# Kernel tuning notes

Hardware: AMD Instinct MI355X
Metric: run time of the kernel (lower is better)

Reference implementation:

```python
import jax, jax.numpy as jnp
import numpy as np
from jax import lax

B, C, H, W = 2, 96, 64, 64
D_INNER, D_STATE, DT_RANK, K = 192, 16, 6, 4
EPS = 1e-5


def _ln(x, g, b):
    mu = jnp.mean(x, -1, keepdims=True)
    var = jnp.var(x, -1, keepdims=True)
    return (x - mu) * lax.rsqrt(var + EPS) * g + b


def setup_inputs() -> dict:
    key = jax.random.key(0)
    ks = jax.random.split(key, 10)
    f = lambda k, s, sc=0.02: jax.random.normal(k, s, dtype=jnp.float32) * sc
    return {
        "rgb": jax.random.normal(ks[0], (B, C, H, W), dtype=jnp.float32),
        "t": jax.random.normal(ks[1], (B, C, H, W), dtype=jnp.float32),
        "conv_w": f(ks[2], (C, 2 * C, 3, 3), 0.05),
        "conv_b": jnp.zeros((C,), jnp.float32),
        "bn_gamma": jnp.ones((C,), jnp.float32),
        "bn_beta": jnp.zeros((C,), jnp.float32),
        "bn_mean": jnp.zeros((C,), jnp.float32),
        "bn_var": jnp.ones((C,), jnp.float32),
        "ln_gamma": jnp.ones((C,), jnp.float32),
        "ln_beta": jnp.zeros((C,), jnp.float32),
        "in_proj_w": f(ks[3], (2 * D_INNER, C)),
        "dwconv_w": f(ks[4], (D_INNER, 1, 3, 3), 0.1),
        "dwconv_b": jnp.zeros((D_INNER,), jnp.float32),
        "x_proj_w": f(ks[5], (K, DT_RANK + 2 * D_STATE, D_INNER)),
        "dt_w": f(ks[6], (K, D_INNER, DT_RANK), 0.1),
        "dt_b": jnp.full((K, D_INNER), float(np.log(np.expm1(0.01))), jnp.float32),
        "A_logs": jnp.log(jnp.tile(jnp.arange(1, D_STATE + 1, dtype=jnp.float32), (K * D_INNER, 1))),
        "Ds": jnp.ones((K * D_INNER,), jnp.float32),
        "out_norm_gamma": jnp.ones((D_INNER,), jnp.float32),
        "out_norm_beta": jnp.zeros((D_INNER,), jnp.float32),
        "out_proj_w": f(ks[7], (C, D_INNER)),
    }


def _forward(rgb, t, conv_w, conv_b, bn_gamma, bn_beta, bn_mean, bn_var,
             ln_gamma, ln_beta, in_proj_w, dwconv_w, dwconv_b, x_proj_w,
             dt_w, dt_b, A_logs, Ds, out_norm_gamma, out_norm_beta, out_proj_w):
    dn = ("NCHW", "OIHW", "NCHW")
    # BasicConv: conv + BN(eval) + ReLU (dropout inactive in eval)
    x = jnp.concatenate([rgb, t], axis=1)
    x = lax.conv_general_dilated(x, conv_w, (1, 1), "SAME", dimension_numbers=dn)
    x = x + conv_b[None, :, None, None]
    x = (x - bn_mean[None, :, None, None]) * lax.rsqrt(bn_var[None, :, None, None] + EPS)
    x = x * bn_gamma[None, :, None, None] + bn_beta[None, :, None, None]
    x = jax.nn.relu(x)
    # permute to (B,H,W,C) and LayerNorm over channels
    x = _ln(jnp.transpose(x, (0, 2, 3, 1)), ln_gamma, ln_beta)
    # ---- SS2D ----
    xz = jnp.einsum("bhwc,ec->bhwe", x, in_proj_w)  # e = 2*d_inner
    xc, z = jnp.split(xz, 2, axis=-1)
    xc = jnp.transpose(xc, (0, 3, 1, 2))  # (B, d_inner, H, W)
    xc = lax.conv_general_dilated(xc, dwconv_w, (1, 1), "SAME",
                                  dimension_numbers=dn, feature_group_count=D_INNER)
    xc = jax.nn.silu(xc + dwconv_b[None, :, None, None])
    L = H * W
    # cross-scan: row-major, col-major, and their reverses -> (B,4,d,L)
    x_flat = xc.reshape(B, D_INNER, L)
    x_tr = jnp.transpose(xc, (0, 1, 3, 2)).reshape(B, D_INNER, L)
    xs = jnp.stack([x_flat, x_tr], axis=1)
    xs = jnp.concatenate([xs, xs[..., ::-1]], axis=1)  # (B,K,d,L)
    x_dbl = jnp.einsum("bkdl,kcd->bkcl", xs, x_proj_w)
    dts = x_dbl[:, :, :DT_RANK]
    Bs = x_dbl[:, :, DT_RANK:DT_RANK + D_STATE]  # (B,K,N,L)
    Cs = x_dbl[:, :, DT_RANK + D_STATE:]         # (B,K,N,L)
    dts = jnp.einsum("bkrl,kdr->bkdl", dts, dt_w)
    A = -jnp.exp(A_logs).reshape(K, D_INNER, D_STATE)
    Dsk = Ds.reshape(K, D_INNER)
    delta = jax.nn.softplus(dts + dt_b[None, :, :, None])  # (B,K,d,L)
    du = delta * xs

    def step(h, inp):
        dl, dul, Bl, Cl = inp  # (B,K,d),(B,K,d),(B,K,N),(B,K,N)
        h = h * jnp.exp(dl[..., None] * A) + dul[..., None] * Bl[:, :, None, :]
        y = jnp.einsum("bkdn,bkn->bkd", h, Cl)
        return h, y

    h0 = jnp.zeros((B, K, D_INNER, D_STATE), delta.dtype)
    _, ys = lax.scan(step, h0, (
        jnp.transpose(delta, (3, 0, 1, 2)),
        jnp.transpose(du, (3, 0, 1, 2)),
        jnp.transpose(Bs, (3, 0, 1, 2)),
        jnp.transpose(Cs, (3, 0, 1, 2)),
    ))
    out_y = jnp.transpose(ys, (1, 2, 3, 0)) + xs * Dsk[None, :, :, None]  # (B,K,d,L)
    # merge four scan directions back to row-major order
    inv_y = out_y[:, 2:4, :, ::-1]
    wh_y = jnp.transpose(out_y[:, 1].reshape(B, D_INNER, W, H), (0, 1, 3, 2)).reshape(B, D_INNER, L)
    invwh_y = jnp.transpose(inv_y[:, 1].reshape(B, D_INNER, W, H), (0, 1, 3, 2)).reshape(B, D_INNER, L)
    y = out_y[:, 0] + inv_y[:, 0] + wh_y + invwh_y  # (B,d,L)
    y = jnp.transpose(y, (0, 2, 1)).reshape(B, H, W, D_INNER)
    y = _ln(y, out_norm_gamma, out_norm_beta)
    y = y * jax.nn.silu(z)
    out = jnp.einsum("bhwd,cd->bhwc", y, out_proj_w)
    return jnp.transpose(out, (0, 3, 1, 2))  # (B,C,H,W)


def reference(rgb, t, conv_w, conv_b, bn_gamma, bn_beta, bn_mean, bn_var,
              ln_gamma, ln_beta, in_proj_w, dwconv_w, dwconv_b, x_proj_w,
              dt_w, dt_b, A_logs, Ds, out_norm_gamma, out_norm_beta, out_proj_w):
    return _forward(rgb, t, conv_w, conv_b, bn_gamma, bn_beta, bn_mean, bn_var,
                    ln_gamma, ln_beta, in_proj_w, dwconv_w, dwconv_b, x_proj_w,
                    dt_w, dt_b, A_logs, Ds, out_norm_gamma, out_norm_beta, out_proj_w)
```

## Files before the change

### kernel.cpp

```cpp
#include <hip/hip_runtime.h>
#include <math.h>

#define HW 4096
#define CC 96
#define DD 192
#define NS 16
#define KK 4
#define LC 64
#define NC 64
#define NCH (8*DD*NS)

__device__ __forceinline__ float siluf(float x){ return x / (1.f + expf(-x)); }
__device__ __forceinline__ float softplusf(float x){ return (x > 20.f) ? x : log1pf(expf(x)); }

__device__ __forceinline__ int lmap_xs(int k, int l){
  if (k == 1) return ((l & 63) << 6) | (l >> 6);
  if (k == 2) return (HW - 1) - l;
  if (k == 3) { int r = (HW - 1) - l; return ((r & 63) << 6) | (r >> 6); }
  return l;
}

__global__ void __launch_bounds__(512, 2)
k_conv1(const float* __restrict__ rgb, const float* __restrict__ tt,
        const float* __restrict__ cw, float* __restrict__ pbuf){
  __shared__ float in_lds[8][10][68];
  __shared__ float w_lds[8][9][48];
  int bi = blockIdx.x;
  int kc  = bi & 7;        int ci0 = kc*24;
  int r2  = bi >> 3;
  int cog = r2 & 1;        int co0 = cog*48;
  int r3  = r2 >> 1;
  int b   = r3 & 1;
  int pt  = r3 >> 1;       int h0 = pt*8;
  int tid = threadIdx.x;
  int pg = tid & 63;  int r = pg >> 3;  int w0 = (pg & 7)*8;
  int cg = tid >> 6;  int co_t = cg*6;

  float acc[6][8];
  #pragma unroll
  for (int c = 0; c < 6; ++c)
    #pragma unroll
    for (int p = 0; p < 8; ++p) acc[c][p] = 0.f;

  for (int s = 0; s < 3; ++s){
    if (s) __syncthreads();
    for (int i = tid; i < 80; i += 512){ in_lds[i/10][i%10][0] = 0.f; in_lds[i/10][i%10][65] = 0.f; }
    for (int i = tid; i < 5120; i += 512){
      int ci = i / 640; int rr = (i % 640) / 64; int w = i & 63;
      int grow = h0 - 1 + rr;
      int cig = ci0 + s*8 + ci;
      float v = 0.f;
      if (grow >= 0 && grow < 64){
        const float* src = (cig < CC) ? (rgb + (size_t)(b*CC+cig)*HW)
                                      : (tt  + (size_t)(b*CC+cig-CC)*HW);
        v = src[grow*64 + w];
      }
      in_lds[ci][rr][w+1] = v;
    }
    for (int i = tid; i < 3456; i += 512){
      int co = i % 48; int rest = i / 48; int ci = rest / 9; int tap = rest % 9;
      int cig = ci0 + s*8 + ci;
      w_lds[ci][tap][co] = cw[((size_t)(co0+co)*192 + cig)*9 + tap];
    }
    __syncthreads();
    #pragma unroll
    for (int ci = 0; ci < 8; ++ci){
      float rowv[3][10];
      #pragma unroll
      for (int rr = 0; rr < 3; ++rr){
        const float* rp = &in_lds[ci][r+rr][w0];
        float4 a = *(const float4*)rp;
        float4 bb = *(const float4*)(rp+4);
        float2 cc = *(const float2*)(rp+8);
        rowv[rr][0]=a.x; rowv[rr][1]=a.y; rowv[rr][2]=a.z; rowv[rr][3]=a.w;
        rowv[rr][4]=bb.x; rowv[rr][5]=bb.y; rowv[rr][6]=bb.z; rowv[rr][7]=bb.w;
        rowv[rr][8]=cc.x; rowv[rr][9]=cc.y;
      }
      #pragma unroll
      for (int tap = 0; tap < 9; ++tap){
        int rt = tap/3, ct = tap - rt*3;
        float2 wa = *(const float2*)&w_lds[ci][tap][co_t];
        float2 wb = *(const float2*)&w_lds[ci][tap][co_t+2];
        float2 wc = *(const float2*)&w_lds[ci][tap][co_t+4];
        float wv[6] = {wa.x, wa.y, wb.x, wb.y, wc.x, wc.y};
        #pragma unroll
        for (int p = 0; p < 8; ++p){
          float iv = rowv[rt][p + ct];
          #pragma unroll
          for (int c = 0; c < 6; ++c) acc[c][p] += wv[c]*iv;
        }
      }
    }
  }
  #pragma unroll
  for (int p = 0; p < 8; ++p){
    int pix = (h0 + r)*64 + w0 + p;
    float* o = pbuf + (((size_t)kc*2 + b)*HW + pix)*CC + co0 + co_t;
    float2 o0 = {acc[0][p], acc[1][p]};
    float2 o1 = {acc[2][p], acc[3][p]};
    float2 o2 = {acc[4][p], acc[5][p]};
    *(float2*)&o[0] = o0; *(float2*)&o[2] = o1; *(float2*)&o[4] = o2;
  }
}

__global__ void k_convred(const float* __restrict__ pbuf, const float* __restrict__ cb,
                          const float* __restrict__ bng, const float* __restrict__ bnb,
                          const float* __restrict__ bnm, const float* __restrict__ bnv,
                          const float* __restrict__ lng, const float* __restrict__ lnb,
                          float* __restrict__ xn){
  __shared__ float sm[4], sm2[4], smu[2], srs[2];
  int tid = threadIdx.x;
  int half = tid >> 7;
  int c = tid & 127;
  int pixg = blockIdx.x*2 + half;
  int b = pixg >> 12; int pix = pixg & (HW-1);
  float v = 0.f;
  if (c < CC){
    #pragma unroll
    for (int kc = 0; kc < 8; ++kc)
      v += pbuf[(((size_t)kc*2 + b)*HW + pix)*CC + c];
    v += cb[c];
    v = (v - bnm[c]) * rsqrtf(bnv[c] + 1e-5f);
    v = v * bng[c] + bnb[c];
    v = fmaxf(v, 0.f);
  }
  float s = v, s2 = v*v;
  #pragma unroll
  for (int off = 32; off; off >>= 1){ s += __shfl_down(s, off); s2 += __shfl_down(s2, off); }
  if ((tid & 63) == 0){ sm[tid>>6] = s; sm2[tid>>6] = s2; }
  __syncthreads();
  if (tid < 2){
    float ts = sm[2*tid] + sm[2*tid+1];
    float ts2 = sm2[2*tid] + sm2[2*tid+1];
    float mu = ts * (1.f/CC);
    float var = ts2 * (1.f/CC) - mu*mu;
    smu[tid] = mu; srs[tid] = rsqrtf(var + 1e-5f);
  }
  __syncthreads();
  if (c < CC)
    xn[(size_t)pixg*CC + c] = (v - smu[half])*srs[half]*lng[c] + lnb[c];
}

__global__ void k_inproj(const float* __restrict__ xn, const float* __restrict__ ipw,
                         float* __restrict__ xz){
  __shared__ float As[64][97];
  __shared__ __align__(16) float Bs[96][68];
  int p0 = blockIdx.x*64;
  int e0 = blockIdx.y*64;
  int tid = threadIdx.x;
  for (int idx = tid; idx < 64*96; idx += 256){
    int r = idx/96, c = idx - r*96;
    As[r][c] = xn[(size_t)(p0+r)*96 + c];
  }
  for (int idx = tid; idx < 96*64; idx += 256){
    int c = idx/64, e = idx - c*64;
    Bs[c][e] = ipw[(size_t)(e0+e)*96 + c];
  }
  __syncthreads();
  int tx = tid & 15, ty = tid >> 4;
  float acc[4][4] = {};
  for (int c = 0; c < 96; ++c){
    float a[4];
    #pragma unroll
    for (int i = 0; i < 4; ++i) a[i] = As[ty*4+i][c];
    float4 bb = *(const float4*)&Bs[c][tx*4];
    float bv[4] = {bb.x, bb.y, bb.z, bb.w};
    #pragma unroll
    for (int i = 0; i < 4; ++i)
      #pragma unroll
      for (int j = 0; j < 4; ++j) acc[i][j] += a[i]*bv[j];
  }
  for (int i = 0; i < 4; ++i){
    float4 o = {acc[i][0], acc[i][1], acc[i][2], acc[i][3]};
    *(float4*)&xz[(size_t)(p0+ty*4+i)*384 + e0 + tx*4] = o;
  }
}

__global__ void k_dwconv(const float* __restrict__ xz, const float* __restrict__ dww,
                         const float* __restrict__ dwb, float* __restrict__ xc){
  int tid = blockIdx.x*256 + threadIdx.x;
  int d  = tid % DD;
  int bp = tid / DD;
  int pix = bp & (HW-1); int b = bp >> 12;
  int h = pix >> 6, w = pix & 63;
  float acc = dwb[d];
  #pragma unroll
  for (int dh = -1; dh <= 1; ++dh){
    int hh = h + dh;
    if (hh < 0 || hh > 63) continue;
    #pragma unroll
    for (int dw = -1; dw <= 1; ++dw){
      int ww = w + dw;
      if (ww < 0 || ww > 63) continue;
      acc += xz[((size_t)b*HW + hh*64 + ww)*384 + d] * dww[d*9 + (dh+1)*3 + (dw+1)];
    }
  }
  xc[(size_t)bp*DD + d] = siluf(acc);
}

__global__ void k_xdbl(const float* __restrict__ xc, const float* __restrict__ xpw,
                       const float* __restrict__ dtw, const float* __restrict__ dtb,
                       float* __restrict__ Bsb, float* __restrict__ Csb,
                       float* __restrict__ dlt){
  __shared__ float xs_t[8][194];
  __shared__ float wl[38*194];
  __shared__ float dts_t[8][38];
  int blk = blockIdx.x;
  int lc = blk & 511; int k = (blk >> 9) & 3; int b = blk >> 11;
  int l0 = lc*8;
  int tid = threadIdx.x;
  for (int idx = tid; idx < 38*192; idx += 256){
    int c = idx/192, d = idx - c*192;
    wl[c*194 + d] = xpw[(size_t)(k*38 + c)*192 + d];
  }
  for (int idx = tid; idx < 8*192; idx += 256){
    int li = idx/192, d = idx - li*192;
    int lm = lmap_xs(k, l0 + li);
    xs_t[li][d] = xc[((size_t)b*HW + lm)*DD + d];
  }
  __syncthreads();
  int b4k = b*KK + k;
  for (int o = tid; o < 8*38; o += 256){
    int li = o/38, c = o - li*38;
    const float* wrow = &wl[c*194];
    float s = 0.f;
    #pragma unroll 4
    for (int d = 0; d < 192; ++d) s += xs_t[li][d]*wrow[d];
    int l = l0 + li;
    if (c < 6)       dts_t[li][c] = s;
    else if (c < 22) Bsb[((size_t)b4k*HW + l)*NS + (c-6)]  = s;
    else             Csb[((size_t)b4k*HW + l)*NS + (c-22)] = s;
  }
  __syncthreads();
  for (int o = tid; o < 8*192; o += 256){
    int li = o/192, d = o - li*192;
    int l = l0 + li;
    float s = dtb[k*DD + d];
    #pragma unroll
    for (int r = 0; r < 6; ++r) s += dts_t[li][r]*dtw[(size_t)(k*DD+d)*6 + r];
    dlt[((size_t)b4k*HW + l)*DD + d] = softplusf(s);
  }
}

__global__ void k_scan1(const float* __restrict__ dlt, const float* __restrict__ xc,
                        const float* __restrict__ Bsb, const float* __restrict__ Alog,
                        float* __restrict__ Ac, float* __restrict__ Bc){
  int tid = blockIdx.x*256 + threadIdx.x;
  int ng = tid & 3;
  int t2 = tid >> 2;
  int d = t2 % DD;
  int rest = t2 / DD;
  int chunk = rest & (NC-1);
  int b4k = rest >> 6;
  int k = b4k & 3, b = b4k >> 2;
  float4 Af = *(const float4*)&Alog[(size_t)(k*DD+d)*NS + ng*4];
  float Av[4] = {-expf(Af.x), -expf(Af.y), -expf(Af.z), -expf(Af.w)};
  float h[4] = {0.f,0.f,0.f,0.f};
  float ap[4] = {1.f,1.f,1.f,1.f};
  int l0 = chunk*LC;
  const float* dp  = dlt + ((size_t)b4k*HW + l0)*DD + d;
  const float4* Bp4 = (const float4*)(Bsb + ((size_t)b4k*HW + l0)*NS) + ng;
  const float* xcb = xc + (size_t)b*HW*DD + d;
  float dvc = dp[0];
  float xvc = xcb[(size_t)lmap_xs(k, l0)*DD];
  float4 Bvc = Bp4[0];
  #pragma unroll 4
  for (int i = 0; i < LC; ++i){
    float dvn = 0.f, xvn = 0.f; float4 Bvn = {0.f,0.f,0.f,0.f};
    if (i+1 < LC){
      dvn = dp[(size_t)(i+1)*DD];
      xvn = xcb[(size_t)lmap_xs(k, l0+i+1)*DD];
      Bvn = Bp4[(size_t)(i+1)*4];
    }
    float du = dvc*xvc;
    float a0 = __expf(dvc*Av[0]), a1 = __expf(dvc*Av[1]),
          a2 = __expf(dvc*Av[2]), a3 = __expf(dvc*Av[3]);
    h[0] = h[0]*a0 + du*Bvc.x; ap[0] *= a0;
    h[1] = h[1]*a1 + du*Bvc.y; ap[1] *= a1;
    h[2] = h[2]*a2 + du*Bvc.z; ap[2] *= a2;
    h[3] = h[3]*a3 + du*Bvc.w; ap[3] *= a3;
    dvc = dvn; xvc = xvn; Bvc = Bvn;
  }
  size_t base = (size_t)chunk*NCH + (size_t)(b4k*DD + d)*NS + ng*4;
  *(float4*)&Ac[base] = make_float4(ap[0],ap[1],ap[2],ap[3]);
  *(float4*)&Bc[base] = make_float4(h[0],h[1],h[2],h[3]);
}

__global__ void k_scan2(float* __restrict__ Ac, const float* __restrict__ Bc){
  int chain = blockIdx.x*256 + threadIdx.x;
  float h = 0.f;
  for (int c = 0; c < NC; ++c){
    size_t idx = (size_t)c*NCH + chain;
    float a = Ac[idx], bv = Bc[idx];
    Ac[idx] = h;
    h = a*h + bv;
  }
}

__global__ void k_scan3(const float* __restrict__ dlt, const float* __restrict__ xc,
                        const float* __restrict__ Bsb, const float* __restrict__ Csb,
                        const float* __restrict__ Alog, const float* __restrict__ hst,
                        float* __restrict__ ys){
  int tid = blockIdx.x*256 + threadIdx.x;
  int ng = tid & 3;
  int t2 = tid >> 2;
  int d = t2 % DD;
  int rest = t2 / DD;
  int chunk = rest & (NC-1);
  int b4k = rest >> 6;
  int k = b4k & 3, b = b4k >> 2;
  float4 Af = *(const float4*)&Alog[(size_t)(k*DD+d)*NS + ng*4];
  float Av[4] = {-expf(Af.x), -expf(Af.y), -expf(Af.z), -expf(Af.w)};
  size_t hbase = (size_t)chunk*NCH + (size_t)(b4k*DD + d)*NS + ng*4;
  float4 hf = *(const float4*)&hst[hbase];
  float h[4] = {hf.x, hf.y, hf.z, hf.w};
  int l0 = chunk*LC;
  const float* dp  = dlt + ((size_t)b4k*HW + l0)*DD + d;
  const float4* Bp4 = (const float4*)(Bsb + ((size_t)b4k*HW + l0)*NS) + ng;
  const float4* Cp4 = (const float4*)(Csb + ((size_t)b4k*HW + l0)*NS) + ng;
  const float* xcb = xc + (size_t)b*HW*DD + d;
  float* yp = ys + ((size_t)b4k*HW + l0)*DD + d;
  float dvc = dp[0];
  float xvc = xcb[(size_t)lmap_xs(k, l0)*DD];
  float4 Bvc = Bp4[0];
  float4 Cvc = Cp4[0];
  #pragma unroll 4
  for (int i = 0; i < LC; ++i){
    float dvn = 0.f, xvn = 0.f; float4 Bvn = {0.f,0.f,0.f,0.f}, Cvn = {0.f,0.f,0.f,0.f};
    if (i+1 < LC){
      dvn = dp[(size_t)(i+1)*DD];
      xvn = xcb[(size_t)lmap_xs(k, l0+i+1)*DD];
      Bvn = Bp4[(size_t)(i+1)*4];
      Cvn = Cp4[(size_t)(i+1)*4];
    }
    float du = dvc*xvc;
    float a0 = __expf(dvc*Av[0]), a1 = __expf(dvc*Av[1]),
          a2 = __expf(dvc*Av[2]), a3 = __expf(dvc*Av[3]);
    h[0] = h[0]*a0 + du*Bvc.x;
    h[1] = h[1]*a1 + du*Bvc.y;
    h[2] = h[2]*a2 + du*Bvc.z;
    h[3] = h[3]*a3 + du*Bvc.w;
    float y = h[0]*Cvc.x + h[1]*Cvc.y + h[2]*Cvc.z + h[3]*Cvc.w;
    y += __shfl_xor(y, 1, 4);
    y += __shfl_xor(y, 2, 4);
    if (ng == 0) yp[(size_t)i*DD] = y;
    dvc = dvn; xvc = xvn; Bvc = Bvn; Cvc = Cvn;
  }
}

__global__ void k_gate(const float* __restrict__ ys, const float* __restrict__ xc,
                       const float* __restrict__ Ds, const float* __restrict__ xz,
                       const float* __restrict__ ong, const float* __restrict__ onb,
                       float* __restrict__ yg){
  int gt = blockIdx.x*256 + threadIdx.x;
  int wave = gt >> 6;
  int lane = gt & 63;
  int b = wave >> 12; int l = wave & (HW-1);
  int l1 = ((l & 63) << 6) | (l >> 6);
  size_t base = (size_t)b*KK*HW*DD;
  float v[3]; float s = 0.f, s2 = 0.f;
  #pragma unroll
  for (int j = 0; j < 3; ++j){
    int d = lane + j*64;
    float t;
    t  = ys[base + ((size_t)0*HW + l        )*DD + d];
    t += ys[base + ((size_t)1*HW + l1       )*DD + d];
    t += ys[base + ((size_t)2*HW + (HW-1-l ))*DD + d];
    t += ys[base + ((size_t)3*HW + (HW-1-l1))*DD + d];
    t += xc[((size_t)b*HW + l)*DD + d] * (Ds[d] + Ds[DD+d] + Ds[2*DD+d] + Ds[3*DD+d]);
    v[j] = t; s += t; s2 += t*t;
  }
  #pragma unroll
  for (int off = 32; off; off >>= 1){ s += __shfl_xor(s, off); s2 += __shfl_xor(s2, off); }
  float mu = s*(1.f/DD);
  float rstd = rsqrtf(s2*(1.f/DD) - mu*mu + 1e-5f);
  #pragma unroll
  for (int j = 0; j < 3; ++j){
    int d = lane + j*64;
    float z = xz[((size_t)b*HW + l)*384 + DD + d];
    float x = (v[j]-mu)*rstd*ong[d] + onb[d];
    yg[(size_t)wave*DD + d] = x * siluf(z);
  }
}

__global__ void k_outproj(const float* __restrict__ yg, const float* __restrict__ opw,
                          float* __restrict__ out){
  __shared__ float yl[48][36];
  __shared__ float wl[48][97];
  int blk = blockIdx.x;
  int b = blk >> 7; int pt = blk & 127;
  int px0 = pt*32;
  int tid = threadIdx.x;
  int pxg = tid & 7;
  int cgi = tid >> 3;
  float acc[4][3] = {};
  for (int k0 = 0; k0 < DD; k0 += 48){
    if (k0) __syncthreads();
    for (int i = tid; i < 32*48; i += 256){
      int r = i/48, k = i - r*48;
      yl[k][r] = yg[((size_t)b*HW + px0 + r)*DD + k0 + k];
    }
    for (int i = tid; i < 96*48; i += 256){
      int c = i/48, k = i - c*48;
      wl[k][c] = opw[(size_t)c*DD + k0 + k];
    }
    __syncthreads();
    #pragma unroll 4
    for (int k = 0; k < 48; ++k){
      float4 yv = *(const float4*)&yl[k][pxg*4];
      float w0 = wl[k][cgi*3], w1 = wl[k][cgi*3+1], w2 = wl[k][cgi*3+2];
      acc[0][0] += yv.x*w0; acc[0][1] += yv.x*w1; acc[0][2] += yv.x*w2;
      acc[1][0] += yv.y*w0; acc[1][1] += yv.y*w1; acc[1][2] += yv.y*w2;
      acc[2][0] += yv.z*w0; acc[2][1] += yv.z*w1; acc[2][2] += yv.z*w2;
      acc[3][0] += yv.w*w0; acc[3][1] += yv.w*w1; acc[3][2] += yv.w*w2;
    }
  }
  #pragma unroll
  for (int j = 0; j < 3; ++j){
    int c = cgi*3 + j;
    float4 o = {acc[0][j], acc[1][j], acc[2][j], acc[3][j]};
    *(float4*)&out[((size_t)b*CC + c)*HW + px0 + pxg*4] = o;
  }
}

extern "C" void kernel_launch(void* const* d_in, const int* in_sizes, int n_in,
                              void* d_out, int out_size, void* d_ws, size_t ws_size,
                              hipStream_t stream) {
  const float* rgb   = (const float*)d_in[0];
  const float* tt    = (const float*)d_in[1];
  const float* cw    = (const float*)d_in[2];
  const float* cb    = (const float*)d_in[3];
  const float* bng   = (const float*)d_in[4];
  const float* bnb   = (const float*)d_in[5];
  const float* bnm   = (const float*)d_in[6];
  const float* bnv   = (const float*)d_in[7];
  const float* lng   = (const float*)d_in[8];
  const float* lnb   = (const float*)d_in[9];
  const float* ipw   = (const float*)d_in[10];
  const float* dww   = (const float*)d_in[11];
  const float* dwb   = (const float*)d_in[12];
  const float* xpw   = (const float*)d_in[13];
  const float* dtw   = (const float*)d_in[14];
  const float* dtb   = (const float*)d_in[15];
  const float* Alog  = (const float*)d_in[16];
  const float* Ds    = (const float*)d_in[17];
  const float* ong   = (const float*)d_in[18];
  const float* onb   = (const float*)d_in[19];
  const float* opw   = (const float*)d_in[20];
  float* out = (float*)d_out;

  float* ws = (float*)d_ws;
  float* xn   = ws + 786432;
  float* xz   = ws + 1572864;
  float* xc   = ws + 4718592;
  float* Bsb  = ws + 6291456;
  float* Csb  = ws + 6815744;
  float* dlt  = ws + 7340032;
  float* ysb  = ws + 13631488;
  float* pbuf = ws + 1572864;
  float* Ac   = ws;
  float* Bc   = ysb;
  float* yg   = ws + 7340032;

  k_conv1<<<256, 512, 0, stream>>>(rgb, tt, cw, pbuf);
  k_convred<<<4096, 256, 0, stream>>>(pbuf, cb, bng, bnb, bnm, bnv, lng, lnb, xn);
  dim3 g2(128, 6);
  k_inproj<<<g2, 256, 0, stream>>>(xn, ipw, xz);
  k_dwconv<<<6144, 256, 0, stream>>>(xz, dww, dwb, xc);
  k_xdbl<<<4096, 256, 0, stream>>>(xc, xpw, dtw, dtb, Bsb, Csb, dlt);
  k_scan1<<<1536, 256, 0, stream>>>(dlt, xc, Bsb, Alog, Ac, Bc);
  k_scan2<<<96, 256, 0, stream>>>(Ac, Bc);
  k_scan3<<<1536, 256, 0, stream>>>(dlt, xc, Bsb, Csb, Alog, Ac, ysb);
  k_gate<<<2048, 256, 0, stream>>>(ysb, xc, Ds, xz, ong, onb, yg);
  k_outproj<<<256, 256, 0, stream>>>(yg, opw, out);
}
```

Baseline: 277.8 us.

## Retile x_proj kernel with register-blocked 32-position tiles and chunked LDS staging

Rewrites the x_proj/dt projection kernel so each block handles 32 sequence positions instead of 8. Each thread computes a 5-channel by 2-position register tile, and the reduction dimension is streamed in 48-wide chunks through transposed LDS buffers loaded with float4. This cuts the per-block reload of the full 38x192 weight matrix and makes better use of each weight load. The dt projection now keeps its dt weights in registers. Block count and size change from 4096x256 to 1024x128, which lowers parallelism per launch.

Result: faster. 258.5 us (-6.9%).

```diff
diff --git a/kernel.cpp b/kernel.cpp
--- a/kernel.cpp
+++ b/kernel.cpp
@@ -198,47 +198,112 @@
   xc[(size_t)bp*DD + d] = siluf(acc);
 }
 
-__global__ void k_xdbl(const float* __restrict__ xc, const float* __restrict__ xpw,
-                       const float* __restrict__ dtw, const float* __restrict__ dtb,
-                       float* __restrict__ Bsb, float* __restrict__ Csb,
-                       float* __restrict__ dlt){
-  __shared__ float xs_t[8][194];
-  __shared__ float wl[38*194];
-  __shared__ float dts_t[8][38];
+__global__ void __launch_bounds__(128)
+k_xdbl(const float* __restrict__ xc, const float* __restrict__ xpw,
+       const float* __restrict__ dtw, const float* __restrict__ dtb,
+       float* __restrict__ Bsb, float* __restrict__ Csb,
+       float* __restrict__ dlt){
+  __shared__ float xs_lds[48*36];
+  __shared__ float w_lds[40*52];
+  __shared__ float dts_lds[32][8];
   int blk = blockIdx.x;
-  int lc = blk & 511; int k = (blk >> 9) & 3; int b = blk >> 11;
-  int l0 = lc*8;
+  int lt = blk & 127; int b4k = blk >> 7;
+  int k = b4k & 3, b = b4k >> 2;
+  int l0 = lt*32;
   int tid = threadIdx.x;
-  for (int idx = tid; idx < 38*192; idx += 256){
-    int c = idx/192, d = idx - c*192;
-    wl[c*194 + d] = xpw[(size_t)(k*38 + c)*192 + d];
-  }
-  for (int idx = tid; idx < 8*192; idx += 256){
-    int li = idx/192, d = idx - li*192;
-    int lm = lmap_xs(k, l0 + li);
-    xs_t[li][d] = xc[((size_t)b*HW + lm)*DD + d];
+  int lg = tid & 15, cg = tid >> 4;
+  int c0 = cg*5;
+  float acc[5][2] = {};
+
+  for (int chunk = 0; chunk < 4; ++chunk){
+    int d0 = chunk*48;
+    if (chunk) __syncthreads();
+    #pragma unroll
+    for (int i = tid; i < 384; i += 128){
+      int q = i >> 5, l = i & 31;
+      int lm = lmap_xs(k, l0 + l);
+      float4 v = *(const float4*)&xc[((size_t)b*HW + lm)*DD + d0 + q*4];
+      xs_lds[(q*4+0)*36 + l] = v.x;
+      xs_lds[(q*4+1)*36 + l] = v.y;
+      xs_lds[(q*4+2)*36 + l] = v.z;
+      xs_lds[(q*4+3)*36 + l] = v.w;
+    }
+    for (int i = tid; i < 456; i += 128){
+      int c = i / 12, q = i - (i/12)*12;
+      float4 v = *(const float4*)&xpw[((size_t)(k*38 + c))*192 + d0 + q*4];
+      *(float4*)&w_lds[c*52 + q*4] = v;
+    }
+    __syncthreads();
+    #pragma unroll 2
+    for (int dq = 0; dq < 12; ++dq){
+      float4 wv[5];
+      #pragma unroll
+      for (int j = 0; j < 5; ++j)
+        wv[j] = *(const float4*)&w_lds[(c0+j)*52 + dq*4];
+      #pragma unroll
+      for (int dd = 0; dd < 4; ++dd){
+        float2 xv = *(const float2*)&xs_lds[(dq*4+dd)*36 + lg*2];
+        #pragma unroll
+        for (int j = 0; j < 5; ++j){
+          float wc = ((const float*)&wv[j])[dd];
+          acc[j][0] += wc * xv.x;
+          acc[j][1] += wc * xv.y;
+        }
+      }
+    }
+  }
+
+  int lA = l0 + lg*2;
+  #pragma unroll
+  for (int j = 0; j < 5; ++j){
+    int c = c0 + j;
+    if (c < 6){
+      dts_lds[lg*2  ][c] = acc[j][0];
+      dts_lds[lg*2+1][c] = acc[j][1];
+    } else if (c < 22){
+      Bsb[((size_t)b4k*HW + lA  )*NS + (c-6)] = acc[j][0];
+      Bsb[((size_t)b4k*HW + lA+1)*NS + (c-6)] = acc[j][1];
+    } else if (c < 38){
+      Csb[((size_t)b4k*HW + lA  )*NS + (c-22)] = acc[j][0];
+      Csb[((size_t)b4k*HW + lA+1)*NS + (c-22)] = acc[j][1];
+    }
   }
   __syncthreads();
-  int b4k = b*KK + k;
-  for (int o = tid; o < 8*38; o += 256){
-    int li = o/38, c = o - li*38;
-    const float* wrow = &wl[c*194];
-    float s = 0.f;
-    #pragma unroll 4
-    for (int d = 0; d < 192; ++d) s += xs_t[li][d]*wrow[d];
-    int l = l0 + li;
-    if (c < 6)       dts_t[li][c] = s;
-    else if (c < 22) Bsb[((size_t)b4k*HW + l)*NS + (c-6)]  = s;
-    else             Csb[((size_t)b4k*HW + l)*NS + (c-22)] = s;
-  }
-  __syncthreads();
-  for (int o = tid; o < 8*192; o += 256){
-    int li = o/192, d = o - li*192;
-    int l = l0 + li;
-    float s = dtb[k*DD + d];
-    #pragma unroll
-    for (int r = 0; r < 6; ++r) s += dts_t[li][r]*dtw[(size_t)(k*DD+d)*6 + r];
-    dlt[((size_t)b4k*HW + l)*DD + d] = softplusf(s);
+
+  float dtw_r0[6], dtw_r1[6], dtw_r2[6];
+  int dv0 = tid % 192, dv1 = (tid + 128) % 192, dv2 = (tid + 256) % 192;
+  float dtb0 = dtb[k*DD + dv0], dtb1 = dtb[k*DD + dv1], dtb2 = dtb[k*DD + dv2];
+  #pragma unroll
+  for (int r = 0; r < 6; ++r){
+    dtw_r0[r] = dtw[((size_t)(k*DD + dv0))*6 + r];
+    dtw_r1[r] = dtw[((size_t)(k*DD + dv1))*6 + r];
+    dtw_r2[r] = dtw[((size_t)(k*DD + dv2))*6 + r];
+  }
+  for (int it3 = 0; it3 < 16; ++it3){
+    {
+      int o = tid + (it3*3+0)*128; int l = o / 192;
+      float4 t0 = *(const float4*)&dts_lds[l][0];
+      float2 t1 = *(const float2*)&dts_lds[l][4];
+      float s = dtb0 + t0.x*dtw_r0[0] + t0.y*dtw_r0[1] + t0.z*dtw_r0[2]
+                     + t0.w*dtw_r0[3] + t1.x*dtw_r0[4] + t1.y*dtw_r0[5];
+      dlt[((size_t)b4k*HW + l0 + l)*DD + dv0] = softplusf(s);
+    }
+    {
+      int o = tid + (it3*3+1)*128; int l = o / 192;
+      float4 t0 = *(const float4*)&dts_lds[l][0];
+      float2 t1 = *(const float2*)&dts_lds[l][4];
+      float s = dtb1 + t0.x*dtw_r1[0] + t0.y*dtw_r1[1] + t0.z*dtw_r1[2]
+                     + t0.w*dtw_r1[3] + t1.x*dtw_r1[4] + t1.y*dtw_r1[5];
+      dlt[((size_t)b4k*HW + l0 + l)*DD + dv1] = softplusf(s);
+    }
+    {
+      int o = tid + (it3*3+2)*128; int l = o / 192;
+      float4 t0 = *(const float4*)&dts_lds[l][0];
+      float2 t1 = *(const float2*)&dts_lds[l][4];
+      float s = dtb2 + t0.x*dtw_r2[0] + t0.y*dtw_r2[1] + t0.z*dtw_r2[2]
+                     + t0.w*dtw_r2[3] + t1.x*dtw_r2[4] + t1.y*dtw_r2[5];
+      dlt[((size_t)b4k*HW + l0 + l)*DD + dv2] = softplusf(s);
+    }
   }
 }
 
@@ -467,7 +532,7 @@
   dim3 g2(128, 6);
   k_inproj<<<g2, 256, 0, stream>>>(xn, ipw, xz);
   k_dwconv<<<6144, 256, 0, stream>>>(xz, dww, dwb, xc);
-  k_xdbl<<<4096, 256, 0, stream>>>(xc, xpw, dtw, dtb, Bsb, Csb, dlt);
+  k_xdbl<<<1024, 128, 0, stream>>>(xc, xpw, dtw, dtb, Bsb, Csb, dlt);
   k_scan1<<<1536, 256, 0, stream>>>(dlt, xc, Bsb, Alog, Ac, Bc);
   k_scan2<<<96, 256, 0, stream>>>(Ac, Bc);
   k_scan3<<<1536, 256, 0, stream>>>(dlt, xc, Bsb, Csb, Alog, Ac, ysb);
```

## Retile x_proj kernel into 64-position blocks with register-blocked 4x4 outer products

Applied to the files above, without the earlier changes.

Rewrites the x_dbl projection kernel so each block handles 64 sequence positions for one (batch, direction) pair instead of 8. The block loads the projection weights in 48-wide chunks into transposed shared memory and computes a 4x4 register tile per thread. The old version reloaded the full 38x192 weight matrix into shared memory for every 8 positions and did scalar dot products. The delta computation now writes contiguous per-position rows and uses a fast exp in softplus, which may slightly change accuracy. Fewer, larger blocks (512 blocks of 192 threads) and about 60KB of shared memory per block could lower occupancy.

Measured after the change: 255.8 us. -7.9%, faster.

```diff
diff --git a/kernel.cpp b/kernel.cpp
--- a/kernel.cpp
+++ b/kernel.cpp
@@ -12,6 +12,7 @@
 
 __device__ __forceinline__ float siluf(float x){ return x / (1.f + expf(-x)); }
 __device__ __forceinline__ float softplusf(float x){ return (x > 20.f) ? x : log1pf(expf(x)); }
+__device__ __forceinline__ float softplus_fast(float x){ return (x > 20.f) ? x : log1pf(__expf(x)); }
 
 __device__ __forceinline__ int lmap_xs(int k, int l){
   if (k == 1) return ((l & 63) << 6) | (l >> 6);
@@ -198,47 +199,95 @@
   xc[(size_t)bp*DD + d] = siluf(acc);
 }
 
-__global__ void k_xdbl(const float* __restrict__ xc, const float* __restrict__ xpw,
-                       const float* __restrict__ dtw, const float* __restrict__ dtb,
-                       float* __restrict__ Bsb, float* __restrict__ Csb,
-                       float* __restrict__ dlt){
-  __shared__ float xs_t[8][194];
-  __shared__ float wl[38*194];
-  __shared__ float dts_t[8][38];
+__global__ void __launch_bounds__(192)
+k_xdbl(const float* __restrict__ xc, const float* __restrict__ xpw,
+       const float* __restrict__ dtw, const float* __restrict__ dtb,
+       float* __restrict__ Bsb, float* __restrict__ Csb,
+       float* __restrict__ dlt){
+  __shared__ float xs_t[192*68];
+  __shared__ float w_t[48*52];
+  __shared__ float dts_s[64][8];
   int blk = blockIdx.x;
-  int lc = blk & 511; int k = (blk >> 9) & 3; int b = blk >> 11;
-  int l0 = lc*8;
+  int lt = blk & 63; int b4k = blk >> 6;
+  int k = b4k & 3, b = b4k >> 2;
+  int l0 = lt*64;
   int tid = threadIdx.x;
-  for (int idx = tid; idx < 38*192; idx += 256){
-    int c = idx/192, d = idx - c*192;
-    wl[c*194 + d] = xpw[(size_t)(k*38 + c)*192 + d];
-  }
-  for (int idx = tid; idx < 8*192; idx += 256){
-    int li = idx/192, d = idx - li*192;
-    int lm = lmap_xs(k, l0 + li);
-    xs_t[li][d] = xc[((size_t)b*HW + lm)*DD + d];
+  int lg = tid & 15, cg = tid >> 4;
+  int c0 = cg*4;
+
+  {
+    int l = tid & 63;
+    int qb = (tid >> 6) * 16;
+    int lm = lmap_xs(k, l0 + l);
+    const float* src = &xc[((size_t)b*HW + lm)*DD];
+    #pragma unroll
+    for (int q = 0; q < 16; ++q){
+      float4 v = *(const float4*)&src[(qb+q)*4];
+      xs_t[((qb+q)*4+0)*68 + l] = v.x;
+      xs_t[((qb+q)*4+1)*68 + l] = v.y;
+      xs_t[((qb+q)*4+2)*68 + l] = v.z;
+      xs_t[((qb+q)*4+3)*68 + l] = v.w;
+    }
+  }
+
+  float acc[4][4] = {};
+  for (int ch = 0; ch < 4; ++ch){
+    __syncthreads();
+    for (int i = tid; i < 456; i += 192){
+      int c = i/12, q = i - (i/12)*12;
+      float4 v = *(const float4*)&xpw[((size_t)(k*38 + c))*192 + ch*48 + q*4];
+      w_t[(q*4+0)*52 + c] = v.x;
+      w_t[(q*4+1)*52 + c] = v.y;
+      w_t[(q*4+2)*52 + c] = v.z;
+      w_t[(q*4+3)*52 + c] = v.w;
+    }
+    __syncthreads();
+    const float* xbase = &xs_t[(ch*48)*68 + lg*4];
+    #pragma unroll 4
+    for (int dd = 0; dd < 48; ++dd){
+      float4 wv = *(const float4*)&w_t[dd*52 + c0];
+      float4 xv = *(const float4*)&xbase[dd*68];
+      acc[0][0] += wv.x*xv.x; acc[0][1] += wv.x*xv.y; acc[0][2] += wv.x*xv.z; acc[0][3] += wv.x*xv.w;
+      acc[1][0] += wv.y*xv.x; acc[1][1] += wv.y*xv.y; acc[1][2] += wv.y*xv.z; acc[1][3] += wv.y*xv.w;
+      acc[2][0] += wv.z*xv.x; acc[2][1] += wv.z*xv.y; acc[2][2] += wv.z*xv.z; acc[2][3] += wv.z*xv.w;
+      acc[3][0] += wv.w*xv.x; acc[3][1] += wv.w*xv.y; acc[3][2] += wv.w*xv.z; acc[3][3] += wv.w*xv.w;
+    }
+  }
+
+  #pragma unroll
+  for (int j = 0; j < 4; ++j){
+    int c = c0 + j;
+    if (c < 6){
+      #pragma unroll
+      for (int i = 0; i < 4; ++i) dts_s[lg*4+i][c] = acc[j][i];
+    } else if (c < 22){
+      #pragma unroll
+      for (int i = 0; i < 4; ++i)
+        Bsb[((size_t)b4k*HW + l0 + lg*4 + i)*NS + (c-6)] = acc[j][i];
+    } else if (c < 38){
+      #pragma unroll
+      for (int i = 0; i < 4; ++i)
+        Csb[((size_t)b4k*HW + l0 + lg*4 + i)*NS + (c-22)] = acc[j][i];
+    }
   }
   __syncthreads();
-  int b4k = b*KK + k;
-  for (int o = tid; o < 8*38; o += 256){
-    int li = o/38, c = o - li*38;
-    const float* wrow = &wl[c*194];
-    float s = 0.f;
+
+  {
+    int l = tid & 63;
+    int dg = tid >> 6;
+    float t0 = dts_s[l][0], t1 = dts_s[l][1], t2 = dts_s[l][2],
+          t3 = dts_s[l][3], t4 = dts_s[l][4], t5 = dts_s[l][5];
+    float* op = &dlt[((size_t)b4k*HW + l0 + l)*DD + dg*64];
+    const float* wp = &dtw[((size_t)(k*DD + dg*64))*6];
+    const float* bp2 = &dtb[k*DD + dg*64];
     #pragma unroll 4
-    for (int d = 0; d < 192; ++d) s += xs_t[li][d]*wrow[d];
-    int l = l0 + li;
-    if (c < 6)       dts_t[li][c] = s;
-    else if (c < 22) Bsb[((size_t)b4k*HW + l)*NS + (c-6)]  = s;
-    else             Csb[((size_t)b4k*HW + l)*NS + (c-22)] = s;
-  }
-  __syncthreads();
-  for (int o = tid; o < 8*192; o += 256){
-    int li = o/192, d = o - li*192;
-    int l = l0 + li;
-    float s = dtb[k*DD + d];
-    #pragma unroll
-    for (int r = 0; r < 6; ++r) s += dts_t[li][r]*dtw[(size_t)(k*DD+d)*6 + r];
-    dlt[((size_t)b4k*HW + l)*DD + d] = softplusf(s);
+    for (int dd = 0; dd < 64; ++dd){
+      float2 wa = *(const float2*)&wp[dd*6];
+      float2 wb = *(const float2*)&wp[dd*6+2];
+      float2 wc = *(const float2*)&wp[dd*6+4];
+      float s = bp2[dd] + t0*wa.x + t1*wa.y + t2*wb.x + t3*wb.y + t4*wc.x + t5*wc.y;
+      op[dd] = softplus_fast(s);
+    }
   }
 }
 
@@ -467,7 +516,7 @@
   dim3 g2(128, 6);
   k_inproj<<<g2, 256, 0, stream>>>(xn, ipw, xz);
   k_dwconv<<<6144, 256, 0, stream>>>(xz, dww, dwb, xc);
-  k_xdbl<<<4096, 256, 0, stream>>>(xc, xpw, dtw, dtb, Bsb, Csb, dlt);
+  k_xdbl<<<512, 192, 0, stream>>>(xc, xpw, dtw, dtb, Bsb, Csb, dlt);
   k_scan1<<<1536, 256, 0, stream>>>(dlt, xc, Bsb, Alog, Ac, Bc);
   k_scan2<<<96, 256, 0, stream>>>(Ac, Bc);
   k_scan3<<<1536, 256, 0, stream>>>(dlt, xc, Bsb, Csb, Alog, Ac, ysb);
```

## Fuse dt projection and softplus into scans, retile x_proj, pre-transpose conv weights

Applied to the files above, without the earlier changes.

The full delta tensor (B*K*L*D_INNER) is no longer materialized. k_xdbl now writes only the 6-wide dt rank vectors, and both scan kernels recompute delta per step from them using a fast-exp softplus. This removes a large write and two large reads. k_xdbl is rewritten as a tiled register-blocked GEMM that handles direction pairs k and k+2 together, since they share the same input with reversed order. Conv1 gets a weight pre-transpose kernel for vectorized weight loads and smaller 256-thread blocks. In exchange, the scans do extra arithmetic per step, and __expf inside softplus slightly changes numerics.

Result: slower. 376.7 us (+35.6%).

```diff
diff --git a/kernel.cpp b/kernel.cpp
--- a/kernel.cpp
+++ b/kernel.cpp
@@ -11,7 +11,7 @@
 #define NCH (8*DD*NS)
 
 __device__ __forceinline__ float siluf(float x){ return x / (1.f + expf(-x)); }
-__device__ __forceinline__ float softplusf(float x){ return (x > 20.f) ? x : log1pf(expf(x)); }
+__device__ __forceinline__ float softplus_fast(float x){ return (x > 20.f) ? x : log1pf(__expf(x)); }
 
 __device__ __forceinline__ int lmap_xs(int k, int l){
   if (k == 1) return ((l & 63) << 6) | (l >> 6);
@@ -20,21 +20,25 @@
   return l;
 }
 
-__global__ void __launch_bounds__(512, 2)
+__global__ void k_wprep(const float* __restrict__ cw, float* __restrict__ wT){
+  int o = blockIdx.x*256 + threadIdx.x;
+  int co = o % 96; int rest = o / 96; int tap = rest % 9; int cig = rest / 9;
+  wT[o] = cw[((size_t)co*192 + cig)*9 + tap];
+}
+
+__global__ void __launch_bounds__(256, 2)
 k_conv1(const float* __restrict__ rgb, const float* __restrict__ tt,
-        const float* __restrict__ cw, float* __restrict__ pbuf){
-  __shared__ float in_lds[8][10][68];
+        const float* __restrict__ wT, float* __restrict__ pbuf){
+  __shared__ float in_lds[8][6][68];
   __shared__ float w_lds[8][9][48];
   int bi = blockIdx.x;
-  int kc  = bi & 7;        int ci0 = kc*24;
-  int r2  = bi >> 3;
-  int cog = r2 & 1;        int co0 = cog*48;
-  int r3  = r2 >> 1;
-  int b   = r3 & 1;
-  int pt  = r3 >> 1;       int h0 = pt*8;
+  int kc  = bi & 7;         int ci0 = kc*24;
+  int cog = (bi >> 3) & 1;  int co0 = cog*48;
+  int b   = (bi >> 4) & 1;
+  int pt  = bi >> 5;        int h0 = pt*4;
   int tid = threadIdx.x;
-  int pg = tid & 63;  int r = pg >> 3;  int w0 = (pg & 7)*8;
-  int cg = tid >> 6;  int co_t = cg*6;
+  int pg = tid & 31;  int r = pg >> 3;  int w0 = (pg & 7)*8;
+  int cg = tid >> 5;  int co_t = cg*6;
 
   float acc[6][8];
   #pragma unroll
@@ -44,9 +48,10 @@
 
   for (int s = 0; s < 3; ++s){
     if (s) __syncthreads();
-    for (int i = tid; i < 80; i += 512){ in_lds[i/10][i%10][0] = 0.f; in_lds[i/10][i%10][65] = 0.f; }
-    for (int i = tid; i < 5120; i += 512){
-      int ci = i / 640; int rr = (i % 640) / 64; int w = i & 63;
+    if (tid < 96){ int side = tid & 1; int rr = (tid>>1)%6; int ci = tid/12;
+                   in_lds[ci][rr][side ? 65 : 0] = 0.f; }
+    for (int i = tid; i < 3072; i += 256){
+      int ci = i / 384; int rem = i - ci*384; int rr = rem >> 6; int w = rem & 63;
       int grow = h0 - 1 + rr;
       int cig = ci0 + s*8 + ci;
       float v = 0.f;
@@ -57,10 +62,10 @@
       }
       in_lds[ci][rr][w+1] = v;
     }
-    for (int i = tid; i < 3456; i += 512){
-      int co = i % 48; int rest = i / 48; int ci = rest / 9; int tap = rest % 9;
-      int cig = ci0 + s*8 + ci;
-      w_lds[ci][tap][co] = cw[((size_t)(co0+co)*192 + cig)*9 + tap];
+    for (int i = tid; i < 864; i += 256){
+      int cq = i % 12; int rest = i / 12; int tap = rest % 9; int ci = rest / 9;
+      float4 v = *(const float4*)&wT[((size_t)(ci0 + s*8 + ci)*9 + tap)*96 + co0 + cq*4];
+      *(float4*)&w_lds[ci][tap][cq*4] = v;
     }
     __syncthreads();
     #pragma unroll
@@ -198,51 +203,70 @@
   xc[(size_t)bp*DD + d] = siluf(acc);
 }
 
-__global__ void k_xdbl(const float* __restrict__ xc, const float* __restrict__ xpw,
-                       const float* __restrict__ dtw, const float* __restrict__ dtb,
-                       float* __restrict__ Bsb, float* __restrict__ Csb,
-                       float* __restrict__ dlt){
-  __shared__ float xs_t[8][194];
-  __shared__ float wl[38*194];
-  __shared__ float dts_t[8][38];
+__global__ void __launch_bounds__(320)
+k_xdbl(const float* __restrict__ xc, const float* __restrict__ xpw,
+       float* __restrict__ Bsb, float* __restrict__ Csb, float* __restrict__ dtsG){
+  __shared__ float xs_t[48*36];
+  __shared__ float w_t[48*80];
   int blk = blockIdx.x;
-  int lc = blk & 511; int k = (blk >> 9) & 3; int b = blk >> 11;
-  int l0 = lc*8;
+  int lt = blk & 127; int p = (blk >> 7) & 1; int b = blk >> 8;
+  int l0 = lt*32;
   int tid = threadIdx.x;
-  for (int idx = tid; idx < 38*192; idx += 256){
-    int c = idx/192, d = idx - c*192;
-    wl[c*194 + d] = xpw[(size_t)(k*38 + c)*192 + d];
-  }
-  for (int idx = tid; idx < 8*192; idx += 256){
-    int li = idx/192, d = idx - li*192;
-    int lm = lmap_xs(k, l0 + li);
-    xs_t[li][d] = xc[((size_t)b*HW + lm)*DD + d];
-  }
-  __syncthreads();
-  int b4k = b*KK + k;
-  for (int o = tid; o < 8*38; o += 256){
-    int li = o/38, c = o - li*38;
-    const float* wrow = &wl[c*194];
-    float s = 0.f;
+  int lg = tid & 15, cg = tid >> 4;
+  int c0 = cg*4;
+  int b4kA = b*4 + p, b4kB = b*4 + p + 2;
+
+  float acc[4][2] = {};
+  for (int ch = 0; ch < 4; ++ch){
+    int d0 = ch*48;
+    if (ch) __syncthreads();
+    for (int i = tid; i < 384; i += 320){
+      int j = i & 31; int dq = i >> 5;
+      int l = l0 + j;
+      int lm = (p == 0) ? l : (((l & 63) << 6) | (l >> 6));
+      float4 v = *(const float4*)&xc[((size_t)b*HW + lm)*DD + d0 + dq*4];
+      xs_t[(dq*4+0)*36 + j] = v.x;
+      xs_t[(dq*4+1)*36 + j] = v.y;
+      xs_t[(dq*4+2)*36 + j] = v.z;
+      xs_t[(dq*4+3)*36 + j] = v.w;
+    }
+    for (int i = tid; i < 3648; i += 320){
+      int c = i % 76; int dd = i / 76;
+      int kk = (c < 38) ? (b4kA & 3) : (b4kB & 3);
+      int cc = (c < 38) ? c : c - 38;
+      w_t[dd*80 + c] = xpw[((size_t)(kk*38 + cc))*192 + d0 + dd];
+    }
+    __syncthreads();
     #pragma unroll 4
-    for (int d = 0; d < 192; ++d) s += xs_t[li][d]*wrow[d];
-    int l = l0 + li;
-    if (c < 6)       dts_t[li][c] = s;
-    else if (c < 22) Bsb[((size_t)b4k*HW + l)*NS + (c-6)]  = s;
-    else             Csb[((size_t)b4k*HW + l)*NS + (c-22)] = s;
-  }
-  __syncthreads();
-  for (int o = tid; o < 8*192; o += 256){
-    int li = o/192, d = o - li*192;
-    int l = l0 + li;
-    float s = dtb[k*DD + d];
-    #pragma unroll
-    for (int r = 0; r < 6; ++r) s += dts_t[li][r]*dtw[(size_t)(k*DD+d)*6 + r];
-    dlt[((size_t)b4k*HW + l)*DD + d] = softplusf(s);
-  }
-}
-
-__global__ void k_scan1(const float* __restrict__ dlt, const float* __restrict__ xc,
+    for (int dd = 0; dd < 48; ++dd){
+      float4 wv = *(const float4*)&w_t[dd*80 + c0];
+      float2 xv = *(const float2*)&xs_t[dd*36 + lg*2];
+      acc[0][0] += wv.x*xv.x; acc[0][1] += wv.x*xv.y;
+      acc[1][0] += wv.y*xv.x; acc[1][1] += wv.y*xv.y;
+      acc[2][0] += wv.z*xv.x; acc[2][1] += wv.z*xv.y;
+      acc[3][0] += wv.w*xv.x; acc[3][1] += wv.w*xv.y;
+    }
+  }
+  #pragma unroll
+  for (int j = 0; j < 4; ++j){
+    int c = c0 + j;
+    #pragma unroll
+    for (int i = 0; i < 2; ++i){
+      float v = acc[j][i];
+      int lf = l0 + lg*2 + i;
+      int lr = HW - 1 - lf;
+      if      (c <  6) dtsG[((size_t)b4kA*HW + lf)*8 + c]        = v;
+      else if (c < 22) Bsb [((size_t)b4kA*HW + lf)*NS + (c-6)]   = v;
+      else if (c < 38) Csb [((size_t)b4kA*HW + lf)*NS + (c-22)]  = v;
+      else if (c < 44) dtsG[((size_t)b4kB*HW + lr)*8 + (c-38)]   = v;
+      else if (c < 60) Bsb [((size_t)b4kB*HW + lr)*NS + (c-44)]  = v;
+      else if (c < 76) Csb [((size_t)b4kB*HW + lr)*NS + (c-60)]  = v;
+    }
+  }
+}
+
+__global__ void k_scan1(const float* __restrict__ dtsG, const float* __restrict__ dtw,
+                        const float* __restrict__ dtb, const float* __restrict__ xc,
                         const float* __restrict__ Bsb, const float* __restrict__ Alog,
                         float* __restrict__ Ac, float* __restrict__ Bc){
   int tid = blockIdx.x*256 + threadIdx.x;
@@ -255,23 +279,36 @@
   int k = b4k & 3, b = b4k >> 2;
   float4 Af = *(const float4*)&Alog[(size_t)(k*DD+d)*NS + ng*4];
   float Av[4] = {-expf(Af.x), -expf(Af.y), -expf(Af.z), -expf(Af.w)};
+  float w6[6];
+  const float* wp = &dtw[(size_t)(k*DD + d)*6];
+  #pragma unroll
+  for (int r = 0; r < 6; ++r) w6[r] = wp[r];
+  float bias = dtb[k*DD + d];
   float h[4] = {0.f,0.f,0.f,0.f};
   float ap[4] = {1.f,1.f,1.f,1.f};
   int l0 = chunk*LC;
-  const float* dp  = dlt + ((size_t)b4k*HW + l0)*DD + d;
+  const float* tp  = dtsG + ((size_t)b4k*HW + l0)*8;
   const float4* Bp4 = (const float4*)(Bsb + ((size_t)b4k*HW + l0)*NS) + ng;
   const float* xcb = xc + (size_t)b*HW*DD + d;
-  float dvc = dp[0];
+  float2 ta = *(const float2*)&tp[0];
+  float2 tb = *(const float2*)&tp[2];
+  float2 tc = *(const float2*)&tp[4];
   float xvc = xcb[(size_t)lmap_xs(k, l0)*DD];
   float4 Bvc = Bp4[0];
   #pragma unroll 4
   for (int i = 0; i < LC; ++i){
-    float dvn = 0.f, xvn = 0.f; float4 Bvn = {0.f,0.f,0.f,0.f};
+    float2 tan={0.f,0.f}, tbn={0.f,0.f}, tcn={0.f,0.f};
+    float xvn = 0.f; float4 Bvn = {0.f,0.f,0.f,0.f};
     if (i+1 < LC){
-      dvn = dp[(size_t)(i+1)*DD];
+      tan = *(const float2*)&tp[(size_t)(i+1)*8];
+      tbn = *(const float2*)&tp[(size_t)(i+1)*8+2];
+      tcn = *(const float2*)&tp[(size_t)(i+1)*8+4];
       xvn = xcb[(size_t)lmap_xs(k, l0+i+1)*DD];
       Bvn = Bp4[(size_t)(i+1)*4];
     }
+    float s = bias + ta.x*w6[0] + ta.y*w6[1] + tb.x*w6[2]
+                   + tb.y*w6[3] + tc.x*w6[4] + tc.y*w6[5];
+    float dvc = softplus_fast(s);
     float du = dvc*xvc;
     float a0 = __expf(dvc*Av[0]), a1 = __expf(dvc*Av[1]),
           a2 = __expf(dvc*Av[2]), a3 = __expf(dvc*Av[3]);
@@ -279,7 +316,7 @@
     h[1] = h[1]*a1 + du*Bvc.y; ap[1] *= a1;
     h[2] = h[2]*a2 + du*Bvc.z; ap[2] *= a2;
     h[3] = h[3]*a3 + du*Bvc.w; ap[3] *= a3;
-    dvc = dvn; xvc = xvn; Bvc = Bvn;
+    ta = tan; tb = tbn; tc = tcn; xvc = xvn; Bvc = Bvn;
   }
   size_t base = (size_t)chunk*NCH + (size_t)(b4k*DD + d)*NS + ng*4;
   *(float4*)&Ac[base] = make_float4(ap[0],ap[1],ap[2],ap[3]);
@@ -297,7 +334,8 @@
   }
 }
 
-__global__ void k_scan3(const float* __restrict__ dlt, const float* __restrict__ xc,
+__global__ void k_scan3(const float* __restrict__ dtsG, const float* __restrict__ dtw,
+                        const float* __restrict__ dtb, const float* __restrict__ xc,
                         const float* __restrict__ Bsb, const float* __restrict__ Csb,
                         const float* __restrict__ Alog, const float* __restrict__ hst,
                         float* __restrict__ ys){
@@ -311,28 +349,41 @@
   int k = b4k & 3, b = b4k >> 2;
   float4 Af = *(const float4*)&Alog[(size_t)(k*DD+d)*NS + ng*4];
   float Av[4] = {-expf(Af.x), -expf(Af.y), -expf(Af.z), -expf(Af.w)};
+  float w6[6];
+  const float* wp = &dtw[(size_t)(k*DD + d)*6];
+  #pragma unroll
+  for (int r = 0; r < 6; ++r) w6[r] = wp[r];
+  float bias = dtb[k*DD + d];
   size_t hbase = (size_t)chunk*NCH + (size_t)(b4k*DD + d)*NS + ng*4;
   float4 hf = *(const float4*)&hst[hbase];
   float h[4] = {hf.x, hf.y, hf.z, hf.w};
   int l0 = chunk*LC;
-  const float* dp  = dlt + ((size_t)b4k*HW + l0)*DD + d;
+  const float* tp  = dtsG + ((size_t)b4k*HW + l0)*8;
   const float4* Bp4 = (const float4*)(Bsb + ((size_t)b4k*HW + l0)*NS) + ng;
   const float4* Cp4 = (const float4*)(Csb + ((size_t)b4k*HW + l0)*NS) + ng;
   const float* xcb = xc + (size_t)b*HW*DD + d;
   float* yp = ys + ((size_t)b4k*HW + l0)*DD + d;
-  float dvc = dp[0];
+  float2 ta = *(const float2*)&tp[0];
+  float2 tb = *(const float2*)&tp[2];
+  float2 tc = *(const float2*)&tp[4];
   float xvc = xcb[(size_t)lmap_xs(k, l0)*DD];
   float4 Bvc = Bp4[0];
   float4 Cvc = Cp4[0];
   #pragma unroll 4
   for (int i = 0; i < LC; ++i){
-    float dvn = 0.f, xvn = 0.f; float4 Bvn = {0.f,0.f,0.f,0.f}, Cvn = {0.f,0.f,0.f,0.f};
+    float2 tan={0.f,0.f}, tbn={0.f,0.f}, tcn={0.f,0.f};
+    float xvn = 0.f; float4 Bvn = {0.f,0.f,0.f,0.f}, Cvn = {0.f,0.f,0.f,0.f};
     if (i+1 < LC){
-      dvn = dp[(size_t)(i+1)*DD];
+      tan = *(const float2*)&tp[(size_t)(i+1)*8];
+      tbn = *(const float2*)&tp[(size_t)(i+1)*8+2];
+      tcn = *(const float2*)&tp[(size_t)(i+1)*8+4];
       xvn = xcb[(size_t)lmap_xs(k, l0+i+1)*DD];
       Bvn = Bp4[(size_t)(i+1)*4];
       Cvn = Cp4[(size_t)(i+1)*4];
     }
+    float s = bias + ta.x*w6[0] + ta.y*w6[1] + tb.x*w6[2]
+                   + tb.y*w6[3] + tc.x*w6[4] + tc.y*w6[5];
+    float dvc = softplus_fast(s);
     float du = dvc*xvc;
     float a0 = __expf(dvc*Av[0]), a1 = __expf(dvc*Av[1]),
           a2 = __expf(dvc*Av[2]), a3 = __expf(dvc*Av[3]);
@@ -344,7 +395,7 @@
     y += __shfl_xor(y, 1, 4);
     y += __shfl_xor(y, 2, 4);
     if (ng == 0) yp[(size_t)i*DD] = y;
-    dvc = dvn; xvc = xvn; Bvc = Bvn; Cvc = Cvn;
+    ta = tan; tb = tbn; tc = tcn; xvc = xvn; Bvc = Bvn; Cvc = Cvn;
   }
 }
 
@@ -455,22 +506,24 @@
   float* xc   = ws + 4718592;
   float* Bsb  = ws + 6291456;
   float* Csb  = ws + 6815744;
-  float* dlt  = ws + 7340032;
+  float* dtsG = ws + 7340032;
+  float* yg   = ws + 7602176;
   float* ysb  = ws + 13631488;
   float* pbuf = ws + 1572864;
   float* Ac   = ws;
   float* Bc   = ysb;
-  float* yg   = ws + 7340032;
-
-  k_conv1<<<256, 512, 0, stream>>>(rgb, tt, cw, pbuf);
+  float* wT   = ws + 16777216;
+
+  k_wprep<<<648, 256, 0, stream>>>(cw, wT);
+  k_conv1<<<512, 256, 0, stream>>>(rgb, tt, wT, pbuf);
   k_convred<<<4096, 256, 0, stream>>>(pbuf, cb, bng, bnb, bnm, bnv, lng, lnb, xn);
   dim3 g2(128, 6);
   k_inproj<<<g2, 256, 0, stream>>>(xn, ipw, xz);
   k_dwconv<<<6144, 256, 0, stream>>>(xz, dww, dwb, xc);
-  k_xdbl<<<4096, 256, 0, stream>>>(xc, xpw, dtw, dtb, Bsb, Csb, dlt);
-  k_scan1<<<1536, 256, 0, stream>>>(dlt, xc, Bsb, Alog, Ac, Bc);
+  k_xdbl<<<512, 320, 0, stream>>>(xc, xpw, Bsb, Csb, dtsG);
+  k_scan1<<<1536, 256, 0, stream>>>(dtsG, dtw, dtb, xc, Bsb, Alog, Ac, Bc);
   k_scan2<<<96, 256, 0, stream>>>(Ac, Bc);
-  k_scan3<<<1536, 256, 0, stream>>>(dlt, xc, Bsb, Csb, Alog, Ac, ysb);
+  k_scan3<<<1536, 256, 0, stream>>>(dtsG, dtw, dtb, xc, Bsb, Csb, Alog, Ac, ysb);
   k_gate<<<2048, 256, 0, stream>>>(ysb, xc, Ds, xz, ong, onb, yg);
   k_outproj<<<256, 256, 0, stream>>>(yg, opw, out);
 }
```
